# Performance work log

Measured on AMD Instinct MI355X. Metric: run time of the kernel, lower is better.

The kernel has to match this reference:

```python
import jax, jax.numpy as jnp
import numpy as np

B, L, D, H, V = 4, 128, 128, 8, 32000
N_ITER = 4
DAMP_H = DAMP_Z = DAMP_X = 0.0
STEP_H = STEP_Z = STEP_X = 1.0
REG_H = REG_Z = REG_X = 1.0
BLOCK_MSG = False
NEG = 1e9


def _norm(t):
    # norm='softmax'
    return jax.nn.softmax(t, axis=-1)


def setup_inputs() -> dict:
    key = jax.random.key(0)
    k1, k2, k3, k4 = jax.random.split(key, 4)
    x = jax.random.normal(k1, (B, L, D), dtype=jnp.float32)
    mask = jnp.ones((B, L), dtype=jnp.int32)
    m_mask = jax.random.randint(k2, (B, L), 0, 2).astype(jnp.int32)
    embed_matrix = jax.random.normal(k3, (V, D), dtype=jnp.float32)
    ternary = jax.random.normal(k4, (2, D, D, H), dtype=jnp.float32)  # dists='' -> 2 groups
    return {"x": x, "mask": mask, "embed_matrix": embed_matrix, "m_mask": m_mask, "ternary": ternary}


def _forward(x, mask, embed_matrix, m_mask, ternary):
    dt = x.dtype
    mask1d = mask != 0                                   # [B,L] True = real token
    valid2d = mask1d[:, :, None] & mask1d[:, None, :]    # [B,L,L]
    inv2d = ~valid2d[:, None, :, :]                      # broadcast over heads
    keep = mask1d[..., None].astype(dt)                  # [B,L,1]
    mm = m_mask.astype(dt)[..., None]                    # [B,L,1]

    # distance mask: dists='' -> [triu(1); tril(-1)] -> [2,L,L]
    dm = jnp.triu(jnp.ones((L, L), dt), 1)
    distmask = jnp.stack([dm, dm.T], axis=0)

    eye = jnp.eye(L, dtype=dt)

    unary = x
    q_x = jnp.ones((B, L, V), dt)
    # initialize_Z=True: masked positions start from expected embedding
    pre = _norm(q_x) @ embed_matrix                      # [B,L,D]
    q_z = unary * (1.0 - mm) + pre * mm
    q_z = q_z * keep

    q_h = jnp.ones((B, H, L, L), dt) - eye * NEG
    q_h = jnp.where(inv2d, -NEG, q_h)

    cache_qh, cache_qz, cache_qx = q_h, q_z, q_x
    # async_update=True: normalize Z before first H update
    q_z = _norm(q_z) * keep

    for _ in range(N_ITER):
        # ---- H update: F[z,c,i,j] = sum_{k,a,b} q_z[z,i,a] q_z[z,j,b] T[k,a,b,c] dist[k,i,j]
        t1 = jnp.einsum('zia,kabc->zkibc', q_z, ternary)            # [B,2,L,D,H]
        F = jnp.einsum('zkibc,zjb,kij->zcij', t1, q_z, distmask)    # [B,H,L,L]
        q_h = cache_qh * DAMP_H + F * (1.0 - DAMP_H) / REG_H
        q_h = cache_qh * (1.0 - STEP_H) + q_h * STEP_H
        cache_qh = q_h
        q_h = q_h - eye * NEG
        q_h = jnp.where(inv2d, -NEG, q_h)
        q_hn = _norm(q_h)                                           # [B,H,L,L]

        # ---- Z update: first-order messages from ternary factors
        m = q_hn[:, None] * distmask[None, :, None]                 # [B,2,H,L,L]
        s1 = jnp.einsum('zkcij,zjb->zkibc', m, q_z)                 # to Z_i (head slot)
        G = jnp.einsum('zkibc,kabc->zia', s1, ternary)
        if not BLOCK_MSG:
            s2 = jnp.einsum('zkcij,zia->zkjac', m, q_z)             # to Z_j (dep slot)
            G = G + jnp.einsum('zkjac,kabc->zjb', s2, ternary)

        # unary: X message replaces word unary at <MASK> positions
        unary_eff = unary * (1.0 - mm) + (_norm(q_x) @ embed_matrix) * mm
        q_z_new = cache_qz * DAMP_Z + (unary_eff + G) * (1.0 - DAMP_Z) / REG_Z
        q_z_new = cache_qz * (1.0 - STEP_Z) + q_z_new * STEP_Z
        cache_qz = q_z_new
        q_z = _norm(q_z_new) * keep

        # ---- X update: message from Z through embedding factor
        msg_x = jnp.einsum('zia,va->ziv', q_z, embed_matrix)        # [B,L,V]
        q_x_new = cache_qx * DAMP_X + msg_x * (1.0 - DAMP_X) / REG_X
        q_x_new = cache_qx * (1.0 - STEP_X) + q_x_new * STEP_X
        cache_qx = q_x_new
        q_x = q_x_new

    # output_prob=False -> unnormalized scores
    return q_x


def reference(x, mask, embed_matrix, m_mask, ternary):
    return _forward(x, mask, embed_matrix, m_mask, ternary)
```

## Files before the change

kernel.cpp:

```cpp
#include <hip/hip_runtime.h>
#include <math.h>

#define L_ 128
#define D_ 128
#define H_ 8
#define V_ 32000
#define NEGC 1e9f

typedef short short8 __attribute__((ext_vector_type(8)));
typedef float f32x4 __attribute__((ext_vector_type(4)));
typedef unsigned short ushort8v __attribute__((ext_vector_type(8)));

__device__ __forceinline__ unsigned short f2bf(float x) {
    unsigned int u = __float_as_uint(x);
    unsigned int r = (u + 0x7fff + ((u >> 16) & 1)) >> 16;
    return (unsigned short)r;
}


__global__ __launch_bounds__(256) void colsum_k(const float* __restrict__ E, float* __restrict__ meansum) {
    int t = threadIdx.x;
    int d = t & 127, h = t >> 7;
    int v0 = blockIdx.x * 256;
    float s = 0.f;
    for (int p = 0; p < 128; ++p)
        s += E[(v0 + h + 2 * p) * 128 + d];
    __shared__ float red[256];
    red[t] = s;
    __syncthreads();
    if (h == 0) atomicAdd(&meansum[d], red[d] + red[128 + d]);
}

__global__ __launch_bounds__(256) void prep_k(const float* __restrict__ E,
                                              unsigned short* __restrict__ Ebf,
                                              unsigned short* __restrict__ Etf,
                                              const float* __restrict__ T, float* __restrict__ Tt,
                                              const int* __restrict__ m_mask,
                                              int* __restrict__ rowidx, int* __restrict__ nactb) {
    __shared__ __align__(16) unsigned char psmem[8704];
    int blk = blockIdx.x;
    int t = threadIdx.x;
    if (blk < 1000) {
        unsigned short* tile = (unsigned short*)psmem;
        int v0 = blk * 32;
#pragma unroll
        for (int i = 0; i < 4; ++i) {
            int idx = i * 256 + t;
            int v = idx >> 5;
            int d4 = (idx & 31) * 4;
            float4 val = *(const float4*)&E[(size_t)(v0 + v) * 128 + d4];
            tile[v * 136 + d4 + 0] = f2bf(val.x);
            tile[v * 136 + d4 + 1] = f2bf(val.y);
            tile[v * 136 + d4 + 2] = f2bf(val.z);
            tile[v * 136 + d4 + 3] = f2bf(val.w);
        }
        __syncthreads();
        {
            int fi = t >> 5;
            int l0 = (t & 31) * 2;
            int vtl = fi >> 2, s = fi & 3;
            size_t base = ((size_t)(blk * 2 + vtl) * 4 + s) * 512;
#pragma unroll
            for (int li = 0; li < 2; ++li) {
                int l = l0 + li;
                int nl = l & 15, hf = l >> 4;
                ushort8v o;
#pragma unroll
                for (int j = 0; j < 8; ++j) o[j] = tile[(vtl * 16 + nl) * 136 + s * 32 + hf * 8 + j];
                *(ushort8v*)&Ebf[base + l * 8] = o;
            }
        }
        {
            int ct = t >> 5;
            int l0 = (t & 31) * 2;
            size_t base = ((size_t)blk * 8 + ct) * 512;
#pragma unroll
            for (int li = 0; li < 2; ++li) {
                int l = l0 + li;
                int nl = l & 15, hf = l >> 4;
                ushort8v o;
#pragma unroll
                for (int j = 0; j < 8; ++j) o[j] = tile[(hf * 8 + j) * 136 + ct * 16 + nl];
                *(ushort8v*)&Etf[base + l * 8] = o;
            }
        }
    } else if (blk < 1256) {
        int tb = blk - 1000;
        for (int q = 0; q < 4; ++q) {
            int id = tb * 1024 + q * 256 + t;
            int k = id >> 17;
            int rem = id & 131071;
            int a = rem >> 10;
            int bc = rem & 1023;
            int b = bc >> 3, c = bc & 7;
            Tt[k * 131072 + b * 1024 + a * 8 + c] = T[id];
        }
    } else {
        int* wc = (int*)psmem;
        bool a0 = m_mask[t] != 0;
        bool a1 = m_mask[t + 256] != 0;
        unsigned long long b0 = __ballot(a0);
        unsigned long long b1 = __ballot(a1);
        int w = t >> 6, lane = t & 63;
        if (lane == 0) { wc[w] = __popcll(b0); wc[4 + w] = __popcll(b1); }
        __syncthreads();
        int base0 = 0;
        for (int i = 0; i < w; ++i) base0 += wc[i];
        int base1 = 0;
        for (int i = 0; i < 4 + w; ++i) base1 += wc[i];
        if (a0) rowidx[base0 + __popcll(b0 & ((1ull << lane) - 1))] = t;
        if (a1) rowidx[base1 + __popcll(b1 & ((1ull << lane) - 1))] = t + 256;
        if (t == 0) {
            int tot = 0;
            for (int i = 0; i < 8; ++i) tot += wc[i];
            nactb[0] = tot;
        }
    }
}

__global__ __launch_bounds__(64) void init_k(const float* __restrict__ x, const int* __restrict__ mask,
                                             const int* __restrict__ m_mask, const float* __restrict__ meansum,
                                             float* __restrict__ ue, float* __restrict__ qz,
                                             unsigned short* __restrict__ qzb) {
    int row = blockIdx.x, t = threadIdx.x;
    float keepv = mask[row] ? 1.f : 0.f;
    bool mm = m_mask[row] != 0;
    float pre0 = meansum[t] * (1.f / 32000.f);
    float pre1 = meansum[t + 64] * (1.f / 32000.f);
    float u0 = mm ? pre0 : x[row * 128 + t];
    float u1 = mm ? pre1 : x[row * 128 + t + 64];
    ue[row * 128 + t] = u0;
    ue[row * 128 + t + 64] = u1;
    float sv0 = u0 * keepv, sv1 = u1 * keepv;
    float m = fmaxf(sv0, sv1);
    for (int off = 32; off; off >>= 1) m = fmaxf(m, __shfl_xor(m, off));
    float e0 = __expf(sv0 - m), e1 = __expf(sv1 - m);
    float s = e0 + e1;
    for (int off = 32; off; off >>= 1) s += __shfl_xor(s, off);
    float inv = keepv / s;
    float q0 = e0 * inv, q1 = e1 * inv;
    qz[row * 128 + t] = q0;
    qz[row * 128 + t + 64] = q1;
    qzb[row * 128 + t] = f2bf(q0);
    qzb[row * 128 + t + 64] = f2bf(q1);
}


__global__ __launch_bounds__(256) void fusedA_k(const float* __restrict__ qz, const float* __restrict__ T,
                                                const float* __restrict__ Tt, float* __restrict__ U2,
                                                unsigned short* __restrict__ Ut, unsigned short* __restrict__ Wt,
                                                const unsigned short* __restrict__ qzb,
                                                const unsigned short* __restrict__ Ebf,
                                                const unsigned short* __restrict__ Etf,
                                                const int* __restrict__ rowidx, const int* __restrict__ nactb,
                                                float* __restrict__ partial, float* __restrict__ partial_rs) {
    __shared__ __align__(16) unsigned char smem[42752];
    int blk = blockIdx.x;
    int t = threadIdx.x;
    if (blk < 512) {
        float* aL = (float*)smem;
        int by = blk >> 5;
        int uw = by >> 3, z = (by >> 1) & 3, k = by & 1;
        int bx = blk & 31;
        int m0 = (bx >> 2) * 16, n = (bx & 3) * 256 + t;
        const float* A = qz + z * 16384;
        const float* Bm = (uw ? Tt : T) + k * 131072;
        for (int idx = t; idx < 2048; idx += 256)
            aL[idx] = A[(m0 + (idx >> 7)) * 128 + (idx & 127)];
        __syncthreads();
        float acc[16];
#pragma unroll
        for (int m = 0; m < 16; ++m) acc[m] = 0.f;
        for (int kq = 0; kq < 32; ++kq) {
            float b0 = Bm[(kq * 4 + 0) * 1024 + n];
            float b1 = Bm[(kq * 4 + 1) * 1024 + n];
            float b2 = Bm[(kq * 4 + 2) * 1024 + n];
            float b3 = Bm[(kq * 4 + 3) * 1024 + n];
#pragma unroll
            for (int m = 0; m < 16; ++m) {
                const float4 aq = *(const float4*)&aL[m * 128 + kq * 4];
                acc[m] += aq.x * b0 + aq.y * b1 + aq.z * b2 + aq.w * b3;
            }
        }
        if (uw == 0) {
            float* Cm = U2 + (z * 2 + k) * 131072;
#pragma unroll
            for (int m = 0; m < 16; ++m)
                Cm[(m0 + m) * 1024 + n] = acc[m];
        }
        int bb = n >> 3, cc = n & 7;
        ushort8v p0, p1;
#pragma unroll
        for (int m = 0; m < 8; ++m) { p0[m] = f2bf(acc[m]); p1[m] = f2bf(acc[8 + m]); }
        unsigned short* To = (uw ? Wt : Ut) + ((size_t)(z * 2 + k) * 128 + bb) * 1024 + cc * 128 + m0;
        *(ushort8v*)&To[0] = p0;
        *(ushort8v*)&To[8] = p1;
    } else {
        int nact = nactb[0];
        int bid = blk - 512;
        int xcd = bid & 7, idx = bid >> 3;
        int g = xcd + 8 * (idx >> 5);
        int bx = idx & 31;
        int r0 = bx * 16;
        if (g >= 50 || r0 >= nact) return;
        unsigned short* Pl = (unsigned short*)smem;
        float* slab = (float*)(smem + 9216);
        float* rsW  = (float*)(smem + 9216 + 33280);
        int w = t >> 6, lane = t & 63;
        int nloc = lane & 15, half = lane >> 4;
        int rA = r0 + nloc;
        bool actA = rA < nact;
        int rowA = actA ? rowidx[rA] : 0;
        short8 zero8 = (short8){0, 0, 0, 0, 0, 0, 0, 0};
        short8 afr[4];
#pragma unroll
        for (int s = 0; s < 4; ++s) {
            short8 v = *(const short8*)&qzb[rowA * 128 + s * 32 + half * 8];
            afr[s] = actA ? v : zero8;
        }
        const int kc0 = g * 20 + w * 5;
        short8 ebb[2][8];
#pragma unroll
        for (int f = 0; f < 8; ++f)
            ebb[0][f] = *(const short8*)&Ebf[((size_t)(kc0 * 8 + f)) * 512 + lane * 8];
        f32x4 acc2[8];
#pragma unroll
        for (int ct = 0; ct < 8; ++ct) acc2[ct] = (f32x4){0.f, 0.f, 0.f, 0.f};
        float rsl = 0.f;
#pragma unroll
        for (int step = 0; step < 5; ++step) {
            const int p = step & 1;
            const int kc = kc0 + step;
            short8 et[8];
#pragma unroll
            for (int f = 0; f < 8; ++f)
                et[f] = *(const short8*)&Etf[((size_t)(kc * 8 + f)) * 512 + lane * 8];
            if (step < 4) {
#pragma unroll
                for (int f = 0; f < 8; ++f)
                    ebb[p ^ 1][f] = *(const short8*)&Ebf[((size_t)((kc + 1) * 8 + f)) * 512 + lane * 8];
            }
            f32x4 p0 = (f32x4){0.f, 0.f, 0.f, 0.f};
            f32x4 p1 = (f32x4){0.f, 0.f, 0.f, 0.f};
#pragma unroll
            for (int s = 0; s < 4; ++s) {
                p0 = __builtin_amdgcn_mfma_f32_16x16x32_bf16(ebb[p][s], afr[s], p0, 0, 0, 0);
                p1 = __builtin_amdgcn_mfma_f32_16x16x32_bf16(ebb[p][4 + s], afr[s], p1, 0, 0, 0);
            }
            unsigned short* pw = Pl + (w * 2 + p) * 576;
            {
                float e0 = __expf(p0[0]), e1 = __expf(p0[1]), e2 = __expf(p0[2]), e3 = __expf(p0[3]);
                rsl += (e0 + e1) + (e2 + e3);
                uint2 pk = {(unsigned)f2bf(e0) | ((unsigned)f2bf(e1) << 16),
                            (unsigned)f2bf(e2) | ((unsigned)f2bf(e3) << 16)};
                *(uint2*)&pw[nloc * 36 + half * 4] = pk;
            }
            {
                float e0 = __expf(p1[0]), e1 = __expf(p1[1]), e2 = __expf(p1[2]), e3 = __expf(p1[3]);
                rsl += (e0 + e1) + (e2 + e3);
                uint2 pk = {(unsigned)f2bf(e0) | ((unsigned)f2bf(e1) << 16),
                            (unsigned)f2bf(e2) | ((unsigned)f2bf(e3) << 16)};
                *(uint2*)&pw[nloc * 36 + 16 + half * 4] = pk;
            }
            short8 a2 = *(const short8*)&pw[nloc * 36 + half * 8];
#pragma unroll
            for (int ct = 0; ct < 8; ++ct)
                acc2[ct] = __builtin_amdgcn_mfma_f32_16x16x32_bf16(a2, et[ct], acc2[ct], 0, 0, 0);
        }
        rsl += __shfl_xor(rsl, 16);
        rsl += __shfl_xor(rsl, 32);
        if (lane < 16) rsW[w * 16 + nloc] = rsl;
#pragma unroll
        for (int ct = 0; ct < 8; ++ct)
#pragma unroll
            for (int reg = 0; reg < 4; ++reg)
                slab[w * 2080 + (half * 4 + reg) * 130 + ct * 16 + nloc] = acc2[ct][reg];
        __syncthreads();
        float* pb = partial + (size_t)g * 65536;
        for (int i = t; i < 2048; i += 256) {
            int row = i >> 7, col = i & 127;
            int rr = r0 + row;
            if (rr < nact)
                pb[rr * 128 + col] = slab[row * 130 + col] + slab[2080 + row * 130 + col]
                                   + slab[4160 + row * 130 + col] + slab[6240 + row * 130 + col];
        }
        if (t < 16) {
            int rr = r0 + t;
            if (rr < nact)
                partial_rs[g * 512 + rr] = rsW[t] + rsW[16 + t] + rsW[32 + t] + rsW[48 + t];
        }
    }
}

__global__ __launch_bounds__(256) void fusedB_k(const float* __restrict__ qz, const float* __restrict__ U2,
                                                const int* __restrict__ mask,
                                                unsigned short* __restrict__ A0b, unsigned short* __restrict__ A1b,
                                                unsigned short* __restrict__ A0Tb, unsigned short* __restrict__ A1Tb,
                                                const float* __restrict__ partial, const float* __restrict__ partial_rs,
                                                const int* __restrict__ rowidx, const int* __restrict__ nactb,
                                                float* __restrict__ exbuf, float* __restrict__ rowsum) {
    __shared__ __align__(16) unsigned char smem[23552];
    int blk = blockIdx.x;
    int t = threadIdx.x;
    if (blk >= 256) {
        int nact = nactb[0];
        int idx = (blk - 256) * 256 + t;
        int rr = idx >> 7, col = idx & 127;
        if (rr >= nact) return;
        float s = 0.f;
#pragma unroll 10
        for (int g = 0; g < 50; ++g)
            s += partial[(size_t)g * 65536 + rr * 128 + col];
        int row = rowidx[rr];
        exbuf[row * 128 + col] = s;
        if (col == 0) {
            float ts = 0.f;
#pragma unroll 10
            for (int g = 0; g < 50; ++g) ts += partial_rs[g * 512 + rr];
            rowsum[row] = ts;
        }
        return;
    }
    float* As = (float*)smem;
    float* Bs = (float*)(smem + 4608);
    int* maskL = (int*)(smem + 4608 + 18432);
    int z = blk >> 6, c = (blk >> 3) & 7, iq = blk & 7;
    int i0 = iq * 16;
    int tj = t & 15, ti = t >> 4;
    int i = i0 + ti;
    if (t < 128) maskL[t] = mask[z * 128 + t];
    float acc0[8], acc1[8];
#pragma unroll
    for (int jj = 0; jj < 8; ++jj) { acc0[jj] = 0.f; acc1[jj] = 0.f; }
    const float* U2z = U2 + (size_t)z * 262144;
    const float* qzz = qz + z * 16384;
    for (int kb = 0; kb < 4; ++kb) {
        int b0 = kb * 32;
        __syncthreads();
        for (int e = t; e < 1024; e += 256) {
            int k = e >> 9, r = e & 511, ii = r >> 5, b = r & 31;
            As[(k * 16 + ii) * 36 + b] = U2z[k * 131072 + (i0 + ii) * 1024 + (b0 + b) * 8 + c];
        }
        for (int f = t; f < 1024; f += 256) {
            int j = f >> 3, b4 = f & 7;
            int slot = b4 ^ ((j >> 3) & 7);
            *(float4*)&Bs[j * 36 + slot * 4] = *(const float4*)&qzz[j * 128 + b0 + b4 * 4];
        }
        __syncthreads();
#pragma unroll
        for (int b4 = 0; b4 < 8; ++b4) {
            float4 a0 = *(const float4*)&As[(0 * 16 + ti) * 36 + b4 * 4];
            float4 a1 = *(const float4*)&As[(1 * 16 + ti) * 36 + b4 * 4];
#pragma unroll
            for (int jj = 0; jj < 8; ++jj) {
                int j = tj * 8 + jj;
                int slot = b4 ^ ((j >> 3) & 7);
                float4 bq = *(const float4*)&Bs[j * 36 + slot * 4];
                acc0[jj] += a0.x * bq.x;
                acc0[jj] += a0.y * bq.y;
                acc0[jj] += a0.z * bq.z;
                acc0[jj] += a0.w * bq.w;
                acc1[jj] += a1.x * bq.x;
                acc1[jj] += a1.y * bq.y;
                acc1[jj] += a1.z * bq.z;
                acc1[jj] += a1.w * bq.w;
            }
        }
    }
    bool vi = maskL[i] != 0;
    float fv[8];
#pragma unroll
    for (int jj = 0; jj < 8; ++jj) {
        int j2 = tj * 8 + jj;
        float F = (j2 > i) ? acc0[jj] : acc1[jj];
        if (j2 == i) F -= NEGC;
        if (!vi || maskL[j2] == 0) F = -NEGC;
        fv[jj] = F;
    }
    float mval = fv[0];
#pragma unroll
    for (int jj = 1; jj < 8; ++jj) mval = fmaxf(mval, fv[jj]);
    for (int off = 1; off < 16; off <<= 1) mval = fmaxf(mval, __shfl_xor(mval, off));
    float ssum = 0.f;
#pragma unroll
    for (int jj = 0; jj < 8; ++jj) ssum += __expf(fv[jj] - mval);
    for (int off = 1; off < 16; off <<= 1) ssum += __shfl_xor(ssum, off);
    float inv = 1.f / ssum;
    size_t base = (size_t)(z * 8 + c) * 16384;
    ushort8v v0, v1;
    unsigned short bvv[8];
#pragma unroll
    for (int jj = 0; jj < 8; ++jj) {
        int j2 = tj * 8 + jj;
        float val = __expf(fv[jj] - mval) * inv;
        unsigned short bv = f2bf(val);
        bvv[jj] = bv;
        v0[jj] = (j2 > i) ? bv : (unsigned short)0;
        v1[jj] = (j2 < i) ? bv : (unsigned short)0;
    }
    *(ushort8v*)&A0b[base + i * 128 + tj * 8] = v0;
    *(ushort8v*)&A1b[base + i * 128 + tj * 8] = v1;
#pragma unroll
    for (int jj = 0; jj < 8; ++jj) {
        int j2 = tj * 8 + jj;
        A0Tb[base + j2 * 128 + i] = (i < j2) ? bvv[jj] : (unsigned short)0;
        A1Tb[base + j2 * 128 + i] = (i > j2) ? bvv[jj] : (unsigned short)0;
    }
}

__global__ __launch_bounds__(64) void gkern_mfma_k(const unsigned short* __restrict__ A0b,
                                                   const unsigned short* __restrict__ A1b,
                                                   const unsigned short* __restrict__ A0Tb,
                                                   const unsigned short* __restrict__ A1Tb,
                                                   const unsigned short* __restrict__ Ut,
                                                   const unsigned short* __restrict__ Wt,
                                                   float* __restrict__ g1, float* __restrict__ g2) {
    int mode = blockIdx.y;
    int bx = blockIdx.x;
    int z = bx >> 6, it = (bx >> 3) & 7, at = bx & 7;
    int lane = threadIdx.x;
    int nloc = lane & 15, half = lane >> 4;
    int i0 = it * 16, a0 = at * 16;
    const unsigned short* Am0 = (mode ? A0Tb : A0b) + (size_t)z * 131072;
    const unsigned short* Am1 = (mode ? A1Tb : A1b) + (size_t)z * 131072;
    const unsigned short* Bt = mode ? Ut : Wt;
    const unsigned short* B0 = Bt + (size_t)(z * 2 + 0) * 131072 + (size_t)(a0 + nloc) * 1024;
    const unsigned short* B1 = Bt + (size_t)(z * 2 + 1) * 131072 + (size_t)(a0 + nloc) * 1024;
    const unsigned short* Ar0 = Am0 + (size_t)(i0 + nloc) * 128;
    const unsigned short* Ar1 = Am1 + (size_t)(i0 + nloc) * 128;
    f32x4 acc = (f32x4){0.f, 0.f, 0.f, 0.f};
#pragma unroll
    for (int c = 0; c < 8; ++c) {
#pragma unroll
        for (int sb = 0; sb < 4; ++sb) {
            int s0 = sb * 32 + half * 8;
            short8 av0 = *(const short8*)&Ar0[c * 16384 + s0];
            short8 bv0 = *(const short8*)&B0[c * 128 + s0];
            acc = __builtin_amdgcn_mfma_f32_16x16x32_bf16(av0, bv0, acc, 0, 0, 0);
            short8 av1 = *(const short8*)&Ar1[c * 16384 + s0];
            short8 bv1 = *(const short8*)&B1[c * 128 + s0];
            acc = __builtin_amdgcn_mfma_f32_16x16x32_bf16(av1, bv1, acc, 0, 0, 0);
        }
    }
    float* G = mode ? g2 : g1;
#pragma unroll
    for (int reg = 0; reg < 4; ++reg)
        G[(z * 128 + i0 + half * 4 + reg) * 128 + a0 + nloc] = acc[reg];
}

__global__ __launch_bounds__(64) void zupd_k(const float* __restrict__ ue, const float* __restrict__ x,
                                             const int* __restrict__ m_mask,
                                             const float* __restrict__ exbuf, const float* __restrict__ rowsum,
                                             const float* __restrict__ g1, const float* __restrict__ g2,
                                             const int* __restrict__ mask,
                                             float* __restrict__ qz, unsigned short* __restrict__ qzb, int useEx) {
    int row = blockIdx.x, t = threadIdx.x;
    float keepv = mask[row] ? 1.f : 0.f;
    int b = row * 128;
    float u0, u1;
    if (useEx) {
        if (m_mask[row] != 0) {
            float rsv = rowsum[row];
            u0 = exbuf[b + t] / rsv;
            u1 = exbuf[b + t + 64] / rsv;
        } else {
            u0 = x[b + t];
            u1 = x[b + t + 64];
        }
    } else {
        u0 = ue[b + t];
        u1 = ue[b + t + 64];
    }
    float v0 = u0 + g1[b + t] + g2[b + t];
    float v1 = u1 + g1[b + t + 64] + g2[b + t + 64];
    float m = fmaxf(v0, v1);
    for (int off = 32; off; off >>= 1) m = fmaxf(m, __shfl_xor(m, off));
    float e0 = __expf(v0 - m), e1 = __expf(v1 - m);
    float s = e0 + e1;
    for (int off = 32; off; off >>= 1) s += __shfl_xor(s, off);
    float inv = keepv / s;
    float q0 = e0 * inv, q1 = e1 * inv;
    qz[b + t] = q0;
    qz[b + t + 64] = q1;
    qzb[b + t] = f2bf(q0);
    qzb[b + t + 64] = f2bf(q1);
}

__global__ __launch_bounds__(256) void msgx_mfma_k(const unsigned short* __restrict__ qzb,
                                                   const unsigned short* __restrict__ Ebf,
                                                   float* __restrict__ out) {
    int t = threadIdx.x;
    int w = t >> 6, lane = t & 63;
    int nloc = lane & 15, half = lane >> 4;
    int rt0 = blockIdx.x * 64;
    int cb0 = blockIdx.y * 256 + w * 64;
    short8 afr[4][4];
#pragma unroll
    for (int r = 0; r < 4; ++r)
#pragma unroll
        for (int s = 0; s < 4; ++s)
            afr[r][s] = *(const short8*)&qzb[(rt0 + r * 16 + nloc) * 128 + s * 32 + half * 8];
    f32x4 acc[4][4];
#pragma unroll
    for (int r = 0; r < 4; ++r)
#pragma unroll
        for (int ct = 0; ct < 4; ++ct)
            acc[r][ct] = (f32x4){0.f, 0.f, 0.f, 0.f};
#pragma unroll
    for (int ct = 0; ct < 4; ++ct) {
#pragma unroll
        for (int s = 0; s < 4; ++s) {
            short8 bfr = *(const short8*)&Ebf[(((size_t)(cb0 >> 4) + ct) * 4 + s) * 512 + lane * 8];
#pragma unroll
            for (int r = 0; r < 4; ++r)
                acc[r][ct] = __builtin_amdgcn_mfma_f32_16x16x32_bf16(afr[r][s], bfr, acc[r][ct], 0, 0, 0);
        }
    }
#pragma unroll
    for (int r = 0; r < 4; ++r)
#pragma unroll
        for (int ct = 0; ct < 4; ++ct) {
            int col = cb0 + ct * 16 + nloc;
#pragma unroll
            for (int reg = 0; reg < 4; ++reg) {
                int row = rt0 + r * 16 + half * 4 + reg;
                out[(size_t)row * V_ + col] = acc[r][ct][reg];
            }
        }
}

extern "C" void kernel_launch(void* const* d_in, const int* in_sizes, int n_in,
                              void* d_out, int out_size, void* d_ws, size_t ws_size,
                              hipStream_t stream) {
    const float* x     = (const float*)d_in[0];
    const int*   mask  = (const int*)d_in[1];
    const float* E     = (const float*)d_in[2];
    const int*   mmask = (const int*)d_in[3];
    const float* T     = (const float*)d_in[4];
    float* out = (float*)d_out;

    float* w = (float*)d_ws;
    float* meansum = w;
    float* ue      = w + 128;
    float* qz      = ue + 65536;
    float* exbuf   = qz + 65536;
    float* rowsum  = exbuf + 65536;
    float* g1      = rowsum + 512;
    float* g2      = g1 + 65536;
    float* Tt      = g2 + 65536;
    float* U2      = Tt + 262144;
    float* prs     = U2 + 1048576;
    unsigned short* qzb  = (unsigned short*)(prs + 25600);
    unsigned short* Ebf  = qzb + 65536;
    unsigned short* Etf  = Ebf + 4096000;
    unsigned short* A0b  = Etf + 4096000;
    unsigned short* A1b  = A0b + 524288;
    unsigned short* A0Tb = A1b + 524288;
    unsigned short* A1Tb = A0Tb + 524288;
    unsigned short* Ut   = A1Tb + 524288;
    unsigned short* Wt   = Ut + 1048576;
    int* rowidx = (int*)(Wt + 1048576);
    int* nactb  = rowidx + 512;

    float* partial = out;

    hipMemsetAsync(meansum, 0, 128 * sizeof(float), stream);
    colsum_k<<<125, 256, 0, stream>>>(E, meansum);
    prep_k<<<1257, 256, 0, stream>>>(E, Ebf, Etf, T, Tt, mmask, rowidx, nactb);
    init_k<<<512, 64, 0, stream>>>(x, mask, mmask, meansum, ue, qz, qzb);

    for (int it = 0; it < 4; ++it) {
        fusedA_k<<<it ? 2304 : 512, 256, 0, stream>>>(qz, T, Tt, U2, Ut, Wt,
                                                      qzb, Ebf, Etf, rowidx, nactb, partial, prs);
        fusedB_k<<<it ? 512 : 256, 256, 0, stream>>>(qz, U2, mask, A0b, A1b, A0Tb, A1Tb,
                                                     partial, prs, rowidx, nactb, exbuf, rowsum);
        gkern_mfma_k<<<dim3(256, 2), 64, 0, stream>>>(A0b, A1b, A0Tb, A1Tb, Ut, Wt, g1, g2);
        zupd_k<<<512, 64, 0, stream>>>(ue, x, mmask, exbuf, rowsum, g1, g2, mask, qz, qzb, it ? 1 : 0);
    }
    msgx_mfma_k<<<dim3(8, 125), 256, 0, stream>>>(qzb, Ebf, out);
}
```

Before: 381.4 us.

## Fuse G message matmul with Z softmax update and fold colsum into prep

```diff
diff --git a/kernel.cpp b/kernel.cpp
--- a/kernel.cpp
+++ b/kernel.cpp
@@ -18,25 +18,13 @@
 }
 
 
-__global__ __launch_bounds__(256) void colsum_k(const float* __restrict__ E, float* __restrict__ meansum) {
-    int t = threadIdx.x;
-    int d = t & 127, h = t >> 7;
-    int v0 = blockIdx.x * 256;
-    float s = 0.f;
-    for (int p = 0; p < 128; ++p)
-        s += E[(v0 + h + 2 * p) * 128 + d];
-    __shared__ float red[256];
-    red[t] = s;
-    __syncthreads();
-    if (h == 0) atomicAdd(&meansum[d], red[d] + red[128 + d]);
-}
-
 __global__ __launch_bounds__(256) void prep_k(const float* __restrict__ E,
                                               unsigned short* __restrict__ Ebf,
                                               unsigned short* __restrict__ Etf,
                                               const float* __restrict__ T, float* __restrict__ Tt,
                                               const int* __restrict__ m_mask,
-                                              int* __restrict__ rowidx, int* __restrict__ nactb) {
+                                              int* __restrict__ rowidx, int* __restrict__ nactb,
+                                              float* __restrict__ meansum) {
     __shared__ __align__(16) unsigned char psmem[8704];
     int blk = blockIdx.x;
     int t = threadIdx.x;
@@ -95,7 +83,7 @@
             int b = bc >> 3, c = bc & 7;
             Tt[k * 131072 + b * 1024 + a * 8 + c] = T[id];
         }
-    } else {
+    } else if (blk == 1256) {
         int* wc = (int*)psmem;
         bool a0 = m_mask[t] != 0;
         bool a1 = m_mask[t + 256] != 0;
@@ -115,6 +103,16 @@
             for (int i = 0; i < 8; ++i) tot += wc[i];
             nactb[0] = tot;
         }
+    } else {
+        float* red = (float*)psmem;
+        int d = t & 127, h = t >> 7;
+        int v0 = (blk - 1257) * 256;
+        float s = 0.f;
+        for (int p = 0; p < 128; ++p)
+            s += E[(size_t)(v0 + h + 2 * p) * 128 + d];
+        red[t] = s;
+        __syncthreads();
+        if (h == 0) atomicAdd(&meansum[d], red[d] + red[128 + d]);
     }
 }
 
@@ -408,82 +406,86 @@
     }
 }
 
-__global__ __launch_bounds__(64) void gkern_mfma_k(const unsigned short* __restrict__ A0b,
-                                                   const unsigned short* __restrict__ A1b,
-                                                   const unsigned short* __restrict__ A0Tb,
-                                                   const unsigned short* __restrict__ A1Tb,
-                                                   const unsigned short* __restrict__ Ut,
-                                                   const unsigned short* __restrict__ Wt,
-                                                   float* __restrict__ g1, float* __restrict__ g2) {
-    int mode = blockIdx.y;
-    int bx = blockIdx.x;
-    int z = bx >> 6, it = (bx >> 3) & 7, at = bx & 7;
-    int lane = threadIdx.x;
+__global__ __launch_bounds__(512) void gkernZ_k(const unsigned short* __restrict__ A0b,
+                                                const unsigned short* __restrict__ A1b,
+                                                const unsigned short* __restrict__ A0Tb,
+                                                const unsigned short* __restrict__ A1Tb,
+                                                const unsigned short* __restrict__ Ut,
+                                                const unsigned short* __restrict__ Wt,
+                                                const float* __restrict__ ue, const float* __restrict__ x,
+                                                const int* __restrict__ m_mask,
+                                                const float* __restrict__ exbuf, const float* __restrict__ rowsum,
+                                                const int* __restrict__ mask,
+                                                float* __restrict__ qz, unsigned short* __restrict__ qzb,
+                                                int useEx) {
+    __shared__ float Gl[2][16][130];
+    int blk = blockIdx.x;
+    int z = blk >> 3, itile = blk & 7;
+    int i0 = itile * 16;
+    int t = threadIdx.x;
+    int w = t >> 6, lane = t & 63;
     int nloc = lane & 15, half = lane >> 4;
-    int i0 = it * 16, a0 = at * 16;
-    const unsigned short* Am0 = (mode ? A0Tb : A0b) + (size_t)z * 131072;
-    const unsigned short* Am1 = (mode ? A1Tb : A1b) + (size_t)z * 131072;
+    int mode = w >> 2;
+    const unsigned short* Ar0 = (mode ? A0Tb : A0b) + (size_t)z * 131072 + (size_t)(i0 + nloc) * 128;
+    const unsigned short* Ar1 = (mode ? A1Tb : A1b) + (size_t)z * 131072 + (size_t)(i0 + nloc) * 128;
     const unsigned short* Bt = mode ? Ut : Wt;
-    const unsigned short* B0 = Bt + (size_t)(z * 2 + 0) * 131072 + (size_t)(a0 + nloc) * 1024;
-    const unsigned short* B1 = Bt + (size_t)(z * 2 + 1) * 131072 + (size_t)(a0 + nloc) * 1024;
-    const unsigned short* Ar0 = Am0 + (size_t)(i0 + nloc) * 128;
-    const unsigned short* Ar1 = Am1 + (size_t)(i0 + nloc) * 128;
-    f32x4 acc = (f32x4){0.f, 0.f, 0.f, 0.f};
-#pragma unroll
-    for (int c = 0; c < 8; ++c) {
-#pragma unroll
-        for (int sb = 0; sb < 4; ++sb) {
-            int s0 = sb * 32 + half * 8;
-            short8 av0 = *(const short8*)&Ar0[c * 16384 + s0];
-            short8 bv0 = *(const short8*)&B0[c * 128 + s0];
-            acc = __builtin_amdgcn_mfma_f32_16x16x32_bf16(av0, bv0, acc, 0, 0, 0);
-            short8 av1 = *(const short8*)&Ar1[c * 16384 + s0];
-            short8 bv1 = *(const short8*)&B1[c * 128 + s0];
-            acc = __builtin_amdgcn_mfma_f32_16x16x32_bf16(av1, bv1, acc, 0, 0, 0);
-        }
-    }
-    float* G = mode ? g2 : g1;
-#pragma unroll
-    for (int reg = 0; reg < 4; ++reg)
-        G[(z * 128 + i0 + half * 4 + reg) * 128 + a0 + nloc] = acc[reg];
-}
-
-__global__ __launch_bounds__(64) void zupd_k(const float* __restrict__ ue, const float* __restrict__ x,
-                                             const int* __restrict__ m_mask,
-                                             const float* __restrict__ exbuf, const float* __restrict__ rowsum,
-                                             const float* __restrict__ g1, const float* __restrict__ g2,
-                                             const int* __restrict__ mask,
-                                             float* __restrict__ qz, unsigned short* __restrict__ qzb, int useEx) {
-    int row = blockIdx.x, t = threadIdx.x;
+#pragma unroll
+    for (int qi = 0; qi < 2; ++qi) {
+        int at = (w & 3) * 2 + qi;
+        int a0 = at * 16;
+        const unsigned short* B0 = Bt + (size_t)(z * 2 + 0) * 131072 + (size_t)(a0 + nloc) * 1024;
+        const unsigned short* B1 = Bt + (size_t)(z * 2 + 1) * 131072 + (size_t)(a0 + nloc) * 1024;
+        f32x4 acc = (f32x4){0.f, 0.f, 0.f, 0.f};
+#pragma unroll
+        for (int c = 0; c < 8; ++c) {
+#pragma unroll
+            for (int sb = 0; sb < 4; ++sb) {
+                int s0 = sb * 32 + half * 8;
+                short8 av0 = *(const short8*)&Ar0[c * 16384 + s0];
+                short8 bv0 = *(const short8*)&B0[c * 128 + s0];
+                acc = __builtin_amdgcn_mfma_f32_16x16x32_bf16(av0, bv0, acc, 0, 0, 0);
+                short8 av1 = *(const short8*)&Ar1[c * 16384 + s0];
+                short8 bv1 = *(const short8*)&B1[c * 128 + s0];
+                acc = __builtin_amdgcn_mfma_f32_16x16x32_bf16(av1, bv1, acc, 0, 0, 0);
+            }
+        }
+#pragma unroll
+        for (int reg = 0; reg < 4; ++reg)
+            Gl[mode][half * 4 + reg][a0 + nloc] = acc[reg];
+    }
+    __syncthreads();
+    int ti = t >> 5, tj = t & 31;
+    int row = z * 128 + i0 + ti;
+    int b = row * 128;
+    int d0 = tj * 4;
     float keepv = mask[row] ? 1.f : 0.f;
-    int b = row * 128;
-    float u0, u1;
+    float4 uu;
     if (useEx) {
         if (m_mask[row] != 0) {
             float rsv = rowsum[row];
-            u0 = exbuf[b + t] / rsv;
-            u1 = exbuf[b + t + 64] / rsv;
+            float4 ex = *(const float4*)&exbuf[b + d0];
+            uu.x = ex.x / rsv; uu.y = ex.y / rsv; uu.z = ex.z / rsv; uu.w = ex.w / rsv;
         } else {
-            u0 = x[b + t];
-            u1 = x[b + t + 64];
+            uu = *(const float4*)&x[b + d0];
         }
     } else {
-        u0 = ue[b + t];
-        u1 = ue[b + t + 64];
-    }
-    float v0 = u0 + g1[b + t] + g2[b + t];
-    float v1 = u1 + g1[b + t + 64] + g2[b + t + 64];
-    float m = fmaxf(v0, v1);
-    for (int off = 32; off; off >>= 1) m = fmaxf(m, __shfl_xor(m, off));
-    float e0 = __expf(v0 - m), e1 = __expf(v1 - m);
-    float s = e0 + e1;
-    for (int off = 32; off; off >>= 1) s += __shfl_xor(s, off);
+        uu = *(const float4*)&ue[b + d0];
+    }
+    float v0 = uu.x + Gl[0][ti][d0 + 0] + Gl[1][ti][d0 + 0];
+    float v1 = uu.y + Gl[0][ti][d0 + 1] + Gl[1][ti][d0 + 1];
+    float v2 = uu.z + Gl[0][ti][d0 + 2] + Gl[1][ti][d0 + 2];
+    float v3 = uu.w + Gl[0][ti][d0 + 3] + Gl[1][ti][d0 + 3];
+    float m = fmaxf(fmaxf(v0, v1), fmaxf(v2, v3));
+    for (int off = 1; off < 32; off <<= 1) m = fmaxf(m, __shfl_xor(m, off));
+    float e0 = __expf(v0 - m), e1 = __expf(v1 - m), e2 = __expf(v2 - m), e3 = __expf(v3 - m);
+    float s = (e0 + e1) + (e2 + e3);
+    for (int off = 1; off < 32; off <<= 1) s += __shfl_xor(s, off);
     float inv = keepv / s;
-    float q0 = e0 * inv, q1 = e1 * inv;
-    qz[b + t] = q0;
-    qz[b + t + 64] = q1;
-    qzb[b + t] = f2bf(q0);
-    qzb[b + t + 64] = f2bf(q1);
+    float4 qv = {e0 * inv, e1 * inv, e2 * inv, e3 * inv};
+    *(float4*)&qz[b + d0] = qv;
+    ushort4 qb;
+    qb.x = f2bf(qv.x); qb.y = f2bf(qv.y); qb.z = f2bf(qv.z); qb.w = f2bf(qv.w);
+    *(ushort4*)&qzb[b + d0] = qb;
 }
 
 __global__ __launch_bounds__(256) void msgx_mfma_k(const unsigned short* __restrict__ qzb,
@@ -545,9 +547,7 @@
     float* qz      = ue + 65536;
     float* exbuf   = qz + 65536;
     float* rowsum  = exbuf + 65536;
-    float* g1      = rowsum + 512;
-    float* g2      = g1 + 65536;
-    float* Tt      = g2 + 65536;
+    float* Tt      = rowsum + 512;
     float* U2      = Tt + 262144;
     float* prs     = U2 + 1048576;
     unsigned short* qzb  = (unsigned short*)(prs + 25600);
@@ -565,8 +565,7 @@
     float* partial = out;
 
     hipMemsetAsync(meansum, 0, 128 * sizeof(float), stream);
-    colsum_k<<<125, 256, 0, stream>>>(E, meansum);
-    prep_k<<<1257, 256, 0, stream>>>(E, Ebf, Etf, T, Tt, mmask, rowidx, nactb);
+    prep_k<<<1382, 256, 0, stream>>>(E, Ebf, Etf, T, Tt, mmask, rowidx, nactb, meansum);
     init_k<<<512, 64, 0, stream>>>(x, mask, mmask, meansum, ue, qz, qzb);
 
     for (int it = 0; it < 4; ++it) {
@@ -574,8 +573,8 @@
                                                       qzb, Ebf, Etf, rowidx, nactb, partial, prs);
         fusedB_k<<<it ? 512 : 256, 256, 0, stream>>>(qz, U2, mask, A0b, A1b, A0Tb, A1Tb,
                                                      partial, prs, rowidx, nactb, exbuf, rowsum);
-        gkern_mfma_k<<<dim3(256, 2), 64, 0, stream>>>(A0b, A1b, A0Tb, A1Tb, Ut, Wt, g1, g2);
-        zupd_k<<<512, 64, 0, stream>>>(ue, x, mmask, exbuf, rowsum, g1, g2, mask, qz, qzb, it ? 1 : 0);
+        gkernZ_k<<<32, 512, 0, stream>>>(A0b, A1b, A0Tb, A1Tb, Ut, Wt,
+                                         ue, x, mmask, exbuf, rowsum, mask, qz, qzb, it ? 1 : 0);
     }
     msgx_mfma_k<<<dim3(8, 125), 256, 0, stream>>>(qzb, Ebf, out);
 }
```

Measured after the change: 561.6 us. +47.3%, slower.
